# Kernel tuning notes

Measured on AMD Instinct MI355X. Metric: run time of the kernel, lower is better.

The kernel has to match this reference:

```python
import jax, jax.numpy as jnp
import numpy as np

V, K, C, F = 100000, 64, 3, 16
HID = [64, 64, 64]  # 'large' pca-net hidden widths (config.yaml stand-in)
EPS = 1e-4


def setup_inputs() -> dict:
    key = jax.random.key(0)
    ks = jax.random.split(key, 12)
    inp = {
        "coordinates": jax.random.normal(ks[0], (V, C), jnp.float32),
        "distsq": jax.random.uniform(ks[1], (V, K), jnp.float32),
        "features": jax.random.uniform(ks[2], (V, F), jnp.float32),
        "n_idxs": jax.random.randint(ks[3], (V, K), 0, V, jnp.int32),
    }
    dims = [C * C] + HID + [C * C]
    for i in range(len(dims) - 1):
        fan_in = dims[i]
        inp[f"W{i}"] = jax.random.normal(ks[4 + 2 * i], (dims[i], dims[i + 1]), jnp.float32) / np.sqrt(fan_in)
        inp[f"b{i}"] = jnp.zeros((dims[i + 1],), jnp.float32)
    return inp


def _neighbour_covariance(coordinates, distsq, features, n_idxs):
    # gather neighbour coords/features: [V,K,C], [V,K,F]
    nbc = jnp.take(coordinates, n_idxs, axis=0)
    nbf = jnp.take(features, n_idxs, axis=0)
    # per-neighbour per-feature weights, distsq pre-scaled by 10 in call()
    w = nbf * jnp.exp(-10.0 * distsq)[:, :, None]          # [V,K,F]
    wsum = jnp.sum(w, axis=1) + EPS                         # [V,F]
    mean = jnp.einsum("vkf,vkc->vfc", w, nbc) / wsum[:, :, None]  # [V,F,C]
    # E[x x^T] - mu mu^T (avoids materializing [V,K,F,C] centered diffs)
    m2 = jnp.einsum("vkf,vkc,vkd->vfcd", w, nbc, nbc) / wsum[:, :, None, None]
    cov = m2 - mean[:, :, :, None] * mean[:, :, None, :]    # [V,F,C,C]
    return cov, mean


def reference(coordinates, distsq, features, n_idxs,
              W0, b0, W1, b1, W2, b2, W3, b3):
    cov, mean = _neighbour_covariance(coordinates, distsq, features, n_idxs)
    x = cov.reshape(-1, C * C)                              # [V*F, C^2]
    # per-layer path: ELU on every layer, including the final one
    for Wl, bl in ((W0, b0), (W1, b1), (W2, b2), (W3, b3)):
        x = jax.nn.elu(x @ Wl + bl)
    return x.reshape(-1, F * C * C)                         # [V, F*C^2]
```

## Files before the change

### kernel.cpp

```cpp
#include <hip/hip_runtime.h>
#include <math.h>

#define NV 100000
#define NK 64
#define NF 16
#define EPS_W 1e-4f
#define WS_NEED ((size_t)NV * 16 * 32)

typedef __attribute__((ext_vector_type(8))) short bf16x8;
typedef __attribute__((ext_vector_type(4))) float f32x4;

__device__ __forceinline__ unsigned int f2bfu(float x) {
    union { float f; unsigned int u; } a; a.f = x;
    return (a.u + 0x7FFFu + ((a.u >> 16) & 1u)) >> 16;
}
__device__ __forceinline__ unsigned int packbf(float lo, float hi) {
    return f2bfu(lo) | (f2bfu(hi) << 16);
}
__device__ __forceinline__ float eluf(float x) {
    return x > 0.f ? x : __expf(x) - 1.f;
}

__launch_bounds__(256)
__global__ void cov_kernel(const float* __restrict__ coords,
                           const float* __restrict__ distsq,
                           const float* __restrict__ feats,
                           const int*   __restrict__ nidx,
                           unsigned char* __restrict__ ws)
{
    __shared__ float sEW[16][64];
    __shared__ int   sIX[16][64];
    const int tid = threadIdx.x;
    const int gv  = tid >> 4;
    const int f   = tid & 15;
    const int v   = blockIdx.x * 16 + gv;

    {
        const size_t base = (size_t)v * NK + 4 * f;
        float4 d4 = *(const float4*)(distsq + base);
        int4   i4 = *(const int4*)(nidx + base);
        sEW[gv][4*f+0] = __expf(-10.f * d4.x);
        sEW[gv][4*f+1] = __expf(-10.f * d4.y);
        sEW[gv][4*f+2] = __expf(-10.f * d4.z);
        sEW[gv][4*f+3] = __expf(-10.f * d4.w);
        sIX[gv][4*f+0] = i4.x; sIX[gv][4*f+1] = i4.y;
        sIX[gv][4*f+2] = i4.z; sIX[gv][4*f+3] = i4.w;
    }
    __syncthreads();

    float s = 0.f, m0=0.f,m1=0.f,m2=0.f;
    float q00=0.f,q01=0.f,q02=0.f,q11=0.f,q12=0.f,q22=0.f;

    #pragma unroll 4
    for (int k = 0; k < NK; ++k) {
        int   idx = sIX[gv][k];
        float ew  = sEW[gv][k];
        float w   = feats[(size_t)idx * NF + f] * ew;
        float x = coords[(size_t)idx*3+0];
        float y = coords[(size_t)idx*3+1];
        float z = coords[(size_t)idx*3+2];
        s += w;
        m0 = fmaf(w,x,m0); m1 = fmaf(w,y,m1); m2 = fmaf(w,z,m2);
        float wx=w*x, wy=w*y, wz=w*z;
        q00=fmaf(wx,x,q00); q01=fmaf(wx,y,q01); q02=fmaf(wx,z,q02);
        q11=fmaf(wy,y,q11); q12=fmaf(wy,z,q12); q22=fmaf(wz,z,q22);
    }
    float inv = 1.f / (s + EPS_W);
    float mu0=m0*inv, mu1=m1*inv, mu2=m2*inv;
    float c00=fmaf(-mu0,mu0,q00*inv);
    float c01=fmaf(-mu0,mu1,q01*inv);
    float c02=fmaf(-mu0,mu2,q02*inv);
    float c11=fmaf(-mu1,mu1,q11*inv);
    float c12=fmaf(-mu1,mu2,q12*inv);
    float c22=fmaf(-mu2,mu2,q22*inv);

    uint4 lo, hi;
    lo.x = packbf(c00, c01);
    lo.y = packbf(c02, c01);
    lo.z = packbf(c11, c12);
    lo.w = packbf(c02, c12);
    hi.x = packbf(c22, 1.0f);
    hi.y = 0u; hi.z = 0u; hi.w = 0u;

    uint4* dst = (uint4*)(ws + ((size_t)v * 16 + f) * 32);
    dst[0] = lo;
    dst[1] = hi;
}

__device__ __forceinline__ bf16x8 rdfrag(const short* hb, int c, int g, int kc) {
    int boff = ((kc << 6) + (g << 4)) ^ ((c & 7) << 4);
    return *(const bf16x8*)(hb + c * 64 + (boff >> 1));
}
__device__ __forceinline__ void wrH(short* hb, int c, int g, int t,
                                    unsigned int p01, unsigned int p23) {
    int boff = ((t << 5) + (g << 3)) ^ ((c & 7) << 4);
    uint2 val; val.x = p01; val.y = p23;
    *(uint2*)(hb + c * 64 + (boff >> 1)) = val;
}

__launch_bounds__(256, 2)
__global__ void mlp_kernel(const unsigned char* __restrict__ ws,
                           const float* __restrict__ W0, const float* __restrict__ b0,
                           const float* __restrict__ W1, const float* __restrict__ b1,
                           const float* __restrict__ W2, const float* __restrict__ b2,
                           const float* __restrict__ W3, const float* __restrict__ b3,
                           float* __restrict__ out)
{
    __shared__ __align__(16) short hbuf[4][16 * 64];
    const int tid  = threadIdx.x;
    const int wid  = tid >> 6;
    const int lane = tid & 63;
    const int c    = lane & 15;
    const int g    = lane >> 4;
    short* hb = &hbuf[wid][0];

    union U8 { short s[8]; bf16x8 v; };

    bf16x8 w0f[4], w1f[8], w2f[8], w3f[2];
    #pragma unroll
    for (int t = 0; t < 4; ++t) {
        U8 u;
        #pragma unroll
        for (int i = 0; i < 8; ++i) {
            int k = 8 * g + i;
            float val = 0.f;
            if (k < 9)       val = W0[k * 64 + 16 * t + c];
            else if (k == 9) val = b0[16 * t + c];
            u.s[i] = (short)f2bfu(val);
        }
        w0f[t] = u.v;
    }
    #pragma unroll
    for (int t = 0; t < 4; ++t) {
        #pragma unroll
        for (int kc = 0; kc < 2; ++kc) {
            U8 u1, u2;
            #pragma unroll
            for (int i = 0; i < 8; ++i) {
                int k = 32 * kc + 8 * g + i;
                u1.s[i] = (short)f2bfu(W1[k * 64 + 16 * t + c]);
                u2.s[i] = (short)f2bfu(W2[k * 64 + 16 * t + c]);
            }
            w1f[2 * t + kc] = u1.v;
            w2f[2 * t + kc] = u2.v;
        }
    }
    #pragma unroll
    for (int kc = 0; kc < 2; ++kc) {
        U8 u;
        #pragma unroll
        for (int i = 0; i < 8; ++i) {
            int k = 32 * kc + 8 * g + i;
            u.s[i] = (short)f2bfu(c < 9 ? W3[k * 9 + c] : 0.f);
        }
        w3f[kc] = u.v;
    }

    float b1v[16], b2v[16], b3v[4];
    #pragma unroll
    for (int t = 0; t < 4; ++t)
        #pragma unroll
        for (int r = 0; r < 4; ++r) {
            b1v[4*t+r] = b1[16*t + 4*g + r];
            b2v[4*t+r] = b2[16*t + 4*g + r];
        }
    #pragma unroll
    for (int r = 0; r < 4; ++r)
        b3v[r] = (4*g + r < 9) ? b3[4*g + r] : 0.f;

    const int stride = gridDim.x * 4;
    for (int t0 = blockIdx.x * 4 + wid; t0 < NV; t0 += stride) {
        f32x4 a[4];
        {
            union { uint4 q; bf16x8 v; } bin;
            bin.q = *(const uint4*)(ws + (size_t)t0 * 512 + (c << 5) + ((g & 1) << 4));
            #pragma unroll
            for (int t = 0; t < 4; ++t) {
                f32x4 z4 = {0.f, 0.f, 0.f, 0.f};
                a[t] = __builtin_amdgcn_mfma_f32_16x16x32_bf16(w0f[t], bin.v, z4, 0, 0, 0);
            }
            #pragma unroll
            for (int t = 0; t < 4; ++t)
                wrH(hb, c, g, t, packbf(eluf(a[t][0]), eluf(a[t][1])),
                                 packbf(eluf(a[t][2]), eluf(a[t][3])));
        }
        {
            bf16x8 h0 = rdfrag(hb, c, g, 0);
            bf16x8 h1 = rdfrag(hb, c, g, 1);
            #pragma unroll
            for (int t = 0; t < 4; ++t) {
                f32x4 acc = { b1v[4*t+0], b1v[4*t+1], b1v[4*t+2], b1v[4*t+3] };
                acc = __builtin_amdgcn_mfma_f32_16x16x32_bf16(w1f[2*t+0], h0, acc, 0, 0, 0);
                acc = __builtin_amdgcn_mfma_f32_16x16x32_bf16(w1f[2*t+1], h1, acc, 0, 0, 0);
                a[t] = acc;
            }
            #pragma unroll
            for (int t = 0; t < 4; ++t)
                wrH(hb, c, g, t, packbf(eluf(a[t][0]), eluf(a[t][1])),
                                 packbf(eluf(a[t][2]), eluf(a[t][3])));
        }
        {
            bf16x8 h0 = rdfrag(hb, c, g, 0);
            bf16x8 h1 = rdfrag(hb, c, g, 1);
            #pragma unroll
            for (int t = 0; t < 4; ++t) {
                f32x4 acc = { b2v[4*t+0], b2v[4*t+1], b2v[4*t+2], b2v[4*t+3] };
                acc = __builtin_amdgcn_mfma_f32_16x16x32_bf16(w2f[2*t+0], h0, acc, 0, 0, 0);
                acc = __builtin_amdgcn_mfma_f32_16x16x32_bf16(w2f[2*t+1], h1, acc, 0, 0, 0);
                a[t] = acc;
            }
            #pragma unroll
            for (int t = 0; t < 4; ++t)
                wrH(hb, c, g, t, packbf(eluf(a[t][0]), eluf(a[t][1])),
                                 packbf(eluf(a[t][2]), eluf(a[t][3])));
        }
        {
            bf16x8 h0 = rdfrag(hb, c, g, 0);
            bf16x8 h1 = rdfrag(hb, c, g, 1);
            f32x4 acc = { b3v[0], b3v[1], b3v[2], b3v[3] };
            acc = __builtin_amdgcn_mfma_f32_16x16x32_bf16(w3f[0], h0, acc, 0, 0, 0);
            acc = __builtin_amdgcn_mfma_f32_16x16x32_bf16(w3f[1], h1, acc, 0, 0, 0);
            float* op = out + (size_t)(t0 * 16 + c) * 9 + (g << 2);
            if (g < 2) {
                op[0] = eluf(acc[0]); op[1] = eluf(acc[1]);
                op[2] = eluf(acc[2]); op[3] = eluf(acc[3]);
            } else if (g == 2) {
                op[0] = eluf(acc[0]);
            }
        }
    }
}

__launch_bounds__(256, 2)
__global__ void fused_pca_mlp(const float* __restrict__ coords,
                              const float* __restrict__ distsq,
                              const float* __restrict__ feats,
                              const int*   __restrict__ nidx,
                              const float* __restrict__ W0, const float* __restrict__ b0,
                              const float* __restrict__ W1, const float* __restrict__ b1,
                              const float* __restrict__ W2, const float* __restrict__ b2,
                              const float* __restrict__ W3, const float* __restrict__ b3,
                              float* __restrict__ out)
{
    __shared__ __align__(16) float sW0t[64 * 9];
    __shared__ __align__(16) float sW1t[64 * 64];
    __shared__ __align__(16) float sW2t[64 * 64];
    __shared__ __align__(16) float sW3t[9 * 64];
    __shared__ float sB0[64], sB1[64], sB2[64], sB3[9];
    const int tid = threadIdx.x;
    for (int t = tid; t < 64 * 9; t += 256) { int j = t / 9, i = t - j * 9; sW0t[t] = W0[i * 64 + j]; }
    for (int t = tid; t < 64 * 64; t += 256) { int j = t >> 6, i = t & 63; sW1t[t] = W1[i * 64 + j]; }
    for (int t = tid; t < 64 * 64; t += 256) { int j = t >> 6, i = t & 63; sW2t[t] = W2[i * 64 + j]; }
    for (int t = tid; t < 9 * 64; t += 256) { int j = t >> 6, i = t & 63; sW3t[t] = W3[i * 9 + j]; }
    if (tid < 64) { sB0[tid] = b0[tid]; sB1[tid] = b1[tid]; sB2[tid] = b2[tid]; }
    if (tid < 9)  { sB3[tid] = b3[tid]; }
    __syncthreads();
    const int g = tid >> 4, f = tid & 15;
    const int v = blockIdx.x * 16 + g;
    if (v >= NV) return;
    const int* nix = nidx + (size_t)v * NK;
    const float* dsq = distsq + (size_t)v * NK;
    float s = 0.f, m0=0,m1=0,m2=0, q00=0,q01=0,q02=0,q11=0,q12=0,q22=0;
    #pragma unroll 4
    for (int k = 0; k < NK; ++k) {
        int idx = nix[k];
        float ew = __expf(-10.0f * dsq[k]);
        float w = feats[(size_t)idx * NF + f] * ew;
        float x = coords[(size_t)idx*3+0], y = coords[(size_t)idx*3+1], z = coords[(size_t)idx*3+2];
        s += w; m0 = fmaf(w,x,m0); m1 = fmaf(w,y,m1); m2 = fmaf(w,z,m2);
        float wx=w*x, wy=w*y, wz=w*z;
        q00=fmaf(wx,x,q00); q01=fmaf(wx,y,q01); q02=fmaf(wx,z,q02);
        q11=fmaf(wy,y,q11); q12=fmaf(wy,z,q12); q22=fmaf(wz,z,q22);
    }
    float inv = 1.0f/(s+EPS_W), mu0=m0*inv, mu1=m1*inv, mu2=m2*inv;
    float xr[9];
    xr[0]=fmaf(-mu0,mu0,q00*inv); xr[1]=fmaf(-mu0,mu1,q01*inv); xr[2]=fmaf(-mu0,mu2,q02*inv);
    xr[3]=xr[1]; xr[4]=fmaf(-mu1,mu1,q11*inv); xr[5]=fmaf(-mu1,mu2,q12*inv);
    xr[6]=xr[2]; xr[7]=xr[5]; xr[8]=fmaf(-mu2,mu2,q22*inv);
    float h[64], gg[64];
    #pragma unroll
    for (int j = 0; j < 64; ++j) {
        float aa = sB0[j]; const float* wr = sW0t + j * 9;
        #pragma unroll
        for (int i = 0; i < 9; ++i) aa = fmaf(xr[i], wr[i], aa);
        h[j] = eluf(aa);
    }
    #pragma unroll
    for (int j = 0; j < 64; ++j) {
        float aa = sB1[j]; const float4* wr = (const float4*)(sW1t + (j << 6));
        #pragma unroll
        for (int i4 = 0; i4 < 16; ++i4) { float4 wv = wr[i4];
            aa = fmaf(h[4*i4+0],wv.x,aa); aa = fmaf(h[4*i4+1],wv.y,aa);
            aa = fmaf(h[4*i4+2],wv.z,aa); aa = fmaf(h[4*i4+3],wv.w,aa); }
        gg[j] = eluf(aa);
    }
    #pragma unroll
    for (int j = 0; j < 64; ++j) {
        float aa = sB2[j]; const float4* wr = (const float4*)(sW2t + (j << 6));
        #pragma unroll
        for (int i4 = 0; i4 < 16; ++i4) { float4 wv = wr[i4];
            aa = fmaf(gg[4*i4+0],wv.x,aa); aa = fmaf(gg[4*i4+1],wv.y,aa);
            aa = fmaf(gg[4*i4+2],wv.z,aa); aa = fmaf(gg[4*i4+3],wv.w,aa); }
        h[j] = eluf(aa);
    }
    float o[9];
    #pragma unroll
    for (int j = 0; j < 9; ++j) {
        float aa = sB3[j]; const float4* wr = (const float4*)(sW3t + (j << 6));
        #pragma unroll
        for (int i4 = 0; i4 < 16; ++i4) { float4 wv = wr[i4];
            aa = fmaf(h[4*i4+0],wv.x,aa); aa = fmaf(h[4*i4+1],wv.y,aa);
            aa = fmaf(h[4*i4+2],wv.z,aa); aa = fmaf(h[4*i4+3],wv.w,aa); }
        o[j] = eluf(aa);
    }
    float* op = out + ((size_t)v * NF + f) * 9;
    #pragma unroll
    for (int j = 0; j < 9; ++j) op[j] = o[j];
}

extern "C" void kernel_launch(void* const* d_in, const int* in_sizes, int n_in,
                              void* d_out, int out_size, void* d_ws, size_t ws_size,
                              hipStream_t stream) {
    (void)in_sizes; (void)n_in; (void)out_size;
    const float* coords = (const float*)d_in[0];
    const float* distsq = (const float*)d_in[1];
    const float* feats  = (const float*)d_in[2];
    const int*   nidx   = (const int*)d_in[3];
    const float* W0 = (const float*)d_in[4];
    const float* b0 = (const float*)d_in[5];
    const float* W1 = (const float*)d_in[6];
    const float* b1 = (const float*)d_in[7];
    const float* W2 = (const float*)d_in[8];
    const float* b2 = (const float*)d_in[9];
    const float* W3 = (const float*)d_in[10];
    const float* b3 = (const float*)d_in[11];
    float* out = (float*)d_out;

    if (ws_size >= WS_NEED) {
        unsigned char* ws = (unsigned char*)d_ws;
        hipLaunchKernelGGL(cov_kernel, dim3(NV / 16), dim3(256), 0, stream,
                           coords, distsq, feats, nidx, ws);
        hipLaunchKernelGGL(mlp_kernel, dim3(1024), dim3(256), 0, stream,
                           ws, W0, b0, W1, b1, W2, b2, W3, b3, out);
    } else {
        hipLaunchKernelGGL(fused_pca_mlp, dim3(NV / 16), dim3(256), 0, stream,
                           coords, distsq, feats, nidx,
                           W0, b0, W1, b1, W2, b2, W3, b3, out);
    }
}
```

Measured before the change: 209.8 us.

## Move MLP hidden weights to LDS and process two vertices per wave

The MLP kernel now stages W1/W2 as swizzled bf16 tiles in shared memory instead of holding them in registers. Each wave processes two vertices per iteration, with separate hidden buffers, so independent MFMA chains can interleave. Biases move to shared memory and are added after the MFMA, the bf16 conversion uses the native __bf16 cast, and the grid grows to 2048 blocks without a min-blocks bound. The aim is lower register pressure and higher occupancy, at the cost of extra LDS reads per layer and explicit lgkmcnt waits.

```diff
diff --git a/kernel.cpp b/kernel.cpp
--- a/kernel.cpp
+++ b/kernel.cpp
@@ -10,12 +10,11 @@
 typedef __attribute__((ext_vector_type(8))) short bf16x8;
 typedef __attribute__((ext_vector_type(4))) float f32x4;
 
-__device__ __forceinline__ unsigned int f2bfu(float x) {
-    union { float f; unsigned int u; } a; a.f = x;
-    return (a.u + 0x7FFFu + ((a.u >> 16) & 1u)) >> 16;
-}
-__device__ __forceinline__ unsigned int packbf(float lo, float hi) {
-    return f2bfu(lo) | (f2bfu(hi) << 16);
+__device__ __forceinline__ unsigned short bfu(float x) {
+    return __builtin_bit_cast(unsigned short, (__bf16)x);
+}
+__device__ __forceinline__ unsigned int pk2(float lo, float hi) {
+    return (unsigned int)bfu(lo) | ((unsigned int)bfu(hi) << 16);
 }
 __device__ __forceinline__ float eluf(float x) {
     return x > 0.f ? x : __expf(x) - 1.f;
@@ -75,11 +74,11 @@
     float c22=fmaf(-mu2,mu2,q22*inv);
 
     uint4 lo, hi;
-    lo.x = packbf(c00, c01);
-    lo.y = packbf(c02, c01);
-    lo.z = packbf(c11, c12);
-    lo.w = packbf(c02, c12);
-    hi.x = packbf(c22, 1.0f);
+    lo.x = pk2(c00, c01);
+    lo.y = pk2(c02, c01);
+    lo.z = pk2(c11, c12);
+    lo.w = pk2(c02, c12);
+    hi.x = pk2(c22, 1.0f);
     hi.y = 0u; hi.z = 0u; hi.w = 0u;
 
     uint4* dst = (uint4*)(ws + ((size_t)v * 16 + f) * 32);
@@ -97,26 +96,52 @@
     uint2 val; val.x = p01; val.y = p23;
     *(uint2*)(hb + c * 64 + (boff >> 1)) = val;
 }
-
-__launch_bounds__(256, 2)
-__global__ void mlp_kernel(const unsigned char* __restrict__ ws,
-                           const float* __restrict__ W0, const float* __restrict__ b0,
-                           const float* __restrict__ W1, const float* __restrict__ b1,
-                           const float* __restrict__ W2, const float* __restrict__ b2,
-                           const float* __restrict__ W3, const float* __restrict__ b3,
-                           float* __restrict__ out)
+__device__ __forceinline__ bf16x8 rdW(const short* sw, int c, int g, int t, int kc) {
+    int byte = (t << 11) + (c << 7) + (kc << 6) + (g << 4);
+    byte ^= (c & 7) << 4;
+    return *(const bf16x8*)((const char*)sw + byte);
+}
+
+__launch_bounds__(256)
+__global__ void mlp3_kernel(const unsigned char* __restrict__ ws,
+                            const float* __restrict__ W0, const float* __restrict__ b0,
+                            const float* __restrict__ W1, const float* __restrict__ b1,
+                            const float* __restrict__ W2, const float* __restrict__ b2,
+                            const float* __restrict__ W3, const float* __restrict__ b3,
+                            float* __restrict__ out)
 {
-    __shared__ __align__(16) short hbuf[4][16 * 64];
+    __shared__ __align__(16) short sW1[4096];
+    __shared__ __align__(16) short sW2[4096];
+    __shared__ float sB1[64], sB2[64], sB3[16];
+    __shared__ __align__(16) short hbuf[4][2][1024];
+
     const int tid  = threadIdx.x;
     const int wid  = tid >> 6;
     const int lane = tid & 63;
     const int c    = lane & 15;
     const int g    = lane >> 4;
-    short* hb = &hbuf[wid][0];
 
     union U8 { short s[8]; bf16x8 v; };
 
-    bf16x8 w0f[4], w1f[8], w2f[8], w3f[2];
+    #pragma unroll
+    for (int r = 0; r < 2; ++r) {
+        int t = tid + r * 256;
+        int j = t & 63, o = t >> 6;
+        U8 u1, u2;
+        #pragma unroll
+        for (int i = 0; i < 8; ++i) {
+            u1.s[i] = (short)bfu(W1[(8 * o + i) * 64 + j]);
+            u2.s[i] = (short)bfu(W2[(8 * o + i) * 64 + j]);
+        }
+        int byte = ((j << 7) + (o << 4)) ^ ((j & 7) << 4);
+        *(bf16x8*)((char*)sW1 + byte) = u1.v;
+        *(bf16x8*)((char*)sW2 + byte) = u2.v;
+    }
+    if (tid < 64) { sB1[tid] = b1[tid]; sB2[tid] = b2[tid]; }
+    if (tid < 16) sB3[tid] = (tid < 9) ? b3[tid] : 0.f;
+    __syncthreads();
+
+    bf16x8 w0f[4], w3f[2];
     #pragma unroll
     for (int t = 0; t < 4; ++t) {
         U8 u;
@@ -126,24 +151,9 @@
             float val = 0.f;
             if (k < 9)       val = W0[k * 64 + 16 * t + c];
             else if (k == 9) val = b0[16 * t + c];
-            u.s[i] = (short)f2bfu(val);
+            u.s[i] = (short)bfu(val);
         }
         w0f[t] = u.v;
-    }
-    #pragma unroll
-    for (int t = 0; t < 4; ++t) {
-        #pragma unroll
-        for (int kc = 0; kc < 2; ++kc) {
-            U8 u1, u2;
-            #pragma unroll
-            for (int i = 0; i < 8; ++i) {
-                int k = 32 * kc + 8 * g + i;
-                u1.s[i] = (short)f2bfu(W1[k * 64 + 16 * t + c]);
-                u2.s[i] = (short)f2bfu(W2[k * 64 + 16 * t + c]);
-            }
-            w1f[2 * t + kc] = u1.v;
-            w2f[2 * t + kc] = u2.v;
-        }
     }
     #pragma unroll
     for (int kc = 0; kc < 2; ++kc) {
@@ -151,81 +161,108 @@
         #pragma unroll
         for (int i = 0; i < 8; ++i) {
             int k = 32 * kc + 8 * g + i;
-            u.s[i] = (short)f2bfu(c < 9 ? W3[k * 9 + c] : 0.f);
+            u.s[i] = (short)bfu(c < 9 ? W3[k * 9 + c] : 0.f);
         }
         w3f[kc] = u.v;
     }
 
-    float b1v[16], b2v[16], b3v[4];
-    #pragma unroll
-    for (int t = 0; t < 4; ++t)
-        #pragma unroll
-        for (int r = 0; r < 4; ++r) {
-            b1v[4*t+r] = b1[16*t + 4*g + r];
-            b2v[4*t+r] = b2[16*t + 4*g + r];
-        }
-    #pragma unroll
-    for (int r = 0; r < 4; ++r)
-        b3v[r] = (4*g + r < 9) ? b3[4*g + r] : 0.f;
-
+    short* hb0 = &hbuf[wid][0][0];
+    short* hb1 = &hbuf[wid][1][0];
+
+    const int npair  = NV / 2;
     const int stride = gridDim.x * 4;
-    for (int t0 = blockIdx.x * 4 + wid; t0 < NV; t0 += stride) {
-        f32x4 a[4];
+    for (int p = blockIdx.x * 4 + wid; p < npair; p += stride) {
+        const int v0 = 2 * p, v1 = 2 * p + 1;
+        f32x4 A0[4], A1[4];
+
         {
-            union { uint4 q; bf16x8 v; } bin;
-            bin.q = *(const uint4*)(ws + (size_t)t0 * 512 + (c << 5) + ((g & 1) << 4));
+            bf16x8 bin0 = *(const bf16x8*)(ws + (size_t)v0 * 512 + (c << 5) + ((g & 1) << 4));
+            bf16x8 bin1 = *(const bf16x8*)(ws + (size_t)v1 * 512 + (c << 5) + ((g & 1) << 4));
             #pragma unroll
             for (int t = 0; t < 4; ++t) {
                 f32x4 z4 = {0.f, 0.f, 0.f, 0.f};
-                a[t] = __builtin_amdgcn_mfma_f32_16x16x32_bf16(w0f[t], bin.v, z4, 0, 0, 0);
-            }
-            #pragma unroll
-            for (int t = 0; t < 4; ++t)
-                wrH(hb, c, g, t, packbf(eluf(a[t][0]), eluf(a[t][1])),
-                                 packbf(eluf(a[t][2]), eluf(a[t][3])));
-        }
+                A0[t] = __builtin_amdgcn_mfma_f32_16x16x32_bf16(w0f[t], bin0, z4, 0, 0, 0);
+                A1[t] = __builtin_amdgcn_mfma_f32_16x16x32_bf16(w0f[t], bin1, z4, 0, 0, 0);
+            }
+            #pragma unroll
+            for (int t = 0; t < 4; ++t) {
+                wrH(hb0, c, g, t, pk2(eluf(A0[t][0]), eluf(A0[t][1])),
+                                  pk2(eluf(A0[t][2]), eluf(A0[t][3])));
+                wrH(hb1, c, g, t, pk2(eluf(A1[t][0]), eluf(A1[t][1])),
+                                  pk2(eluf(A1[t][2]), eluf(A1[t][3])));
+            }
+        }
+        __asm__ volatile("s_waitcnt lgkmcnt(0)" ::: "memory");
+
         {
-            bf16x8 h0 = rdfrag(hb, c, g, 0);
-            bf16x8 h1 = rdfrag(hb, c, g, 1);
-            #pragma unroll
-            for (int t = 0; t < 4; ++t) {
-                f32x4 acc = { b1v[4*t+0], b1v[4*t+1], b1v[4*t+2], b1v[4*t+3] };
-                acc = __builtin_amdgcn_mfma_f32_16x16x32_bf16(w1f[2*t+0], h0, acc, 0, 0, 0);
-                acc = __builtin_amdgcn_mfma_f32_16x16x32_bf16(w1f[2*t+1], h1, acc, 0, 0, 0);
-                a[t] = acc;
-            }
-            #pragma unroll
-            for (int t = 0; t < 4; ++t)
-                wrH(hb, c, g, t, packbf(eluf(a[t][0]), eluf(a[t][1])),
-                                 packbf(eluf(a[t][2]), eluf(a[t][3])));
-        }
+            bf16x8 h00 = rdfrag(hb0, c, g, 0), h01 = rdfrag(hb0, c, g, 1);
+            bf16x8 h10 = rdfrag(hb1, c, g, 0), h11 = rdfrag(hb1, c, g, 1);
+            #pragma unroll
+            for (int t = 0; t < 4; ++t) {
+                bf16x8 wa = rdW(sW1, c, g, t, 0);
+                bf16x8 wb = rdW(sW1, c, g, t, 1);
+                f32x4 z4 = {0.f, 0.f, 0.f, 0.f};
+                f32x4 a0 = __builtin_amdgcn_mfma_f32_16x16x32_bf16(wa, h00, z4, 0, 0, 0);
+                a0       = __builtin_amdgcn_mfma_f32_16x16x32_bf16(wb, h01, a0, 0, 0, 0);
+                f32x4 a1 = __builtin_amdgcn_mfma_f32_16x16x32_bf16(wa, h10, z4, 0, 0, 0);
+                a1       = __builtin_amdgcn_mfma_f32_16x16x32_bf16(wb, h11, a1, 0, 0, 0);
+                A0[t] = a0; A1[t] = a1;
+            }
+            #pragma unroll
+            for (int t = 0; t < 4; ++t) {
+                float4 bb = *(const float4*)(sB1 + 16 * t + 4 * g);
+                wrH(hb0, c, g, t, pk2(eluf(A0[t][0] + bb.x), eluf(A0[t][1] + bb.y)),
+                                  pk2(eluf(A0[t][2] + bb.z), eluf(A0[t][3] + bb.w)));
+                wrH(hb1, c, g, t, pk2(eluf(A1[t][0] + bb.x), eluf(A1[t][1] + bb.y)),
+                                  pk2(eluf(A1[t][2] + bb.z), eluf(A1[t][3] + bb.w)));
+            }
+        }
+        __asm__ volatile("s_waitcnt lgkmcnt(0)" ::: "memory");
+
         {
-            bf16x8 h0 = rdfrag(hb, c, g, 0);
-            bf16x8 h1 = rdfrag(hb, c, g, 1);
-            #pragma unroll
-            for (int t = 0; t < 4; ++t) {
-                f32x4 acc = { b2v[4*t+0], b2v[4*t+1], b2v[4*t+2], b2v[4*t+3] };
-                acc = __builtin_amdgcn_mfma_f32_16x16x32_bf16(w2f[2*t+0], h0, acc, 0, 0, 0);
-                acc = __builtin_amdgcn_mfma_f32_16x16x32_bf16(w2f[2*t+1], h1, acc, 0, 0, 0);
-                a[t] = acc;
-            }
-            #pragma unroll
-            for (int t = 0; t < 4; ++t)
-                wrH(hb, c, g, t, packbf(eluf(a[t][0]), eluf(a[t][1])),
-                                 packbf(eluf(a[t][2]), eluf(a[t][3])));
-        }
+            bf16x8 h00 = rdfrag(hb0, c, g, 0), h01 = rdfrag(hb0, c, g, 1);
+            bf16x8 h10 = rdfrag(hb1, c, g, 0), h11 = rdfrag(hb1, c, g, 1);
+            #pragma unroll
+            for (int t = 0; t < 4; ++t) {
+                bf16x8 wa = rdW(sW2, c, g, t, 0);
+                bf16x8 wb = rdW(sW2, c, g, t, 1);
+                f32x4 z4 = {0.f, 0.f, 0.f, 0.f};
+                f32x4 a0 = __builtin_amdgcn_mfma_f32_16x16x32_bf16(wa, h00, z4, 0, 0, 0);
+                a0       = __builtin_amdgcn_mfma_f32_16x16x32_bf16(wb, h01, a0, 0, 0, 0);
+                f32x4 a1 = __builtin_amdgcn_mfma_f32_16x16x32_bf16(wa, h10, z4, 0, 0, 0);
+                a1       = __builtin_amdgcn_mfma_f32_16x16x32_bf16(wb, h11, a1, 0, 0, 0);
+                A0[t] = a0; A1[t] = a1;
+            }
+            #pragma unroll
+            for (int t = 0; t < 4; ++t) {
+                float4 bb = *(const float4*)(sB2 + 16 * t + 4 * g);
+                wrH(hb0, c, g, t, pk2(eluf(A0[t][0] + bb.x), eluf(A0[t][1] + bb.y)),
+                                  pk2(eluf(A0[t][2] + bb.z), eluf(A0[t][3] + bb.w)));
+                wrH(hb1, c, g, t, pk2(eluf(A1[t][0] + bb.x), eluf(A1[t][1] + bb.y)),
+                                  pk2(eluf(A1[t][2] + bb.z), eluf(A1[t][3] + bb.w)));
+            }
+        }
+        __asm__ volatile("s_waitcnt lgkmcnt(0)" ::: "memory");
+
         {
-            bf16x8 h0 = rdfrag(hb, c, g, 0);
-            bf16x8 h1 = rdfrag(hb, c, g, 1);
-            f32x4 acc = { b3v[0], b3v[1], b3v[2], b3v[3] };
-            acc = __builtin_amdgcn_mfma_f32_16x16x32_bf16(w3f[0], h0, acc, 0, 0, 0);
-            acc = __builtin_amdgcn_mfma_f32_16x16x32_bf16(w3f[1], h1, acc, 0, 0, 0);
-            float* op = out + (size_t)(t0 * 16 + c) * 9 + (g << 2);
+            bf16x8 h00 = rdfrag(hb0, c, g, 0), h01 = rdfrag(hb0, c, g, 1);
+            bf16x8 h10 = rdfrag(hb1, c, g, 0), h11 = rdfrag(hb1, c, g, 1);
+            f32x4 z4 = {0.f, 0.f, 0.f, 0.f};
+            f32x4 a0 = __builtin_amdgcn_mfma_f32_16x16x32_bf16(w3f[0], h00, z4, 0, 0, 0);
+            a0       = __builtin_amdgcn_mfma_f32_16x16x32_bf16(w3f[1], h01, a0, 0, 0, 0);
+            f32x4 a1 = __builtin_amdgcn_mfma_f32_16x16x32_bf16(w3f[0], h10, z4, 0, 0, 0);
+            a1       = __builtin_amdgcn_mfma_f32_16x16x32_bf16(w3f[1], h11, a1, 0, 0, 0);
+            float4 bb = *(const float4*)(sB3 + 4 * g);
+            float* op0 = out + (size_t)(v0 * 16 + c) * 9 + (g << 2);
+            float* op1 = out + (size_t)(v1 * 16 + c) * 9 + (g << 2);
             if (g < 2) {
-                op[0] = eluf(acc[0]); op[1] = eluf(acc[1]);
-                op[2] = eluf(acc[2]); op[3] = eluf(acc[3]);
+                op0[0] = eluf(a0[0] + bb.x); op0[1] = eluf(a0[1] + bb.y);
+                op0[2] = eluf(a0[2] + bb.z); op0[3] = eluf(a0[3] + bb.w);
+                op1[0] = eluf(a1[0] + bb.x); op1[1] = eluf(a1[1] + bb.y);
+                op1[2] = eluf(a1[2] + bb.z); op1[3] = eluf(a1[3] + bb.w);
             } else if (g == 2) {
-                op[0] = eluf(acc[0]);
+                op0[0] = eluf(a0[0] + bb.x);
+                op1[0] = eluf(a1[0] + bb.x);
             }
         }
     }
@@ -340,7 +377,7 @@
         unsigned char* ws = (unsigned char*)d_ws;
         hipLaunchKernelGGL(cov_kernel, dim3(NV / 16), dim3(256), 0, stream,
                            coords, distsq, feats, nidx, ws);
-        hipLaunchKernelGGL(mlp_kernel, dim3(1024), dim3(256), 0, stream,
+        hipLaunchKernelGGL(mlp3_kernel, dim3(2048), dim3(256), 0, stream,
                            ws, W0, b0, W1, b1, W2, b2, W3, b3, out);
     } else {
         hipLaunchKernelGGL(fused_pca_mlp, dim3(NV / 16), dim3(256), 0, stream,
```

Result: faster. 200.7 us (-4.3%).
